# Kernel tuning notes

Measured on AMD Instinct MI355X. Metric: run time of the kernel, lower is better.

Reference implementation:

```python
import jax, jax.numpy as jnp
import numpy as np

SEG_NUM = 100000
D_SEG = 128
D_S = 258       # 2*D_SEG + 2 (offset)
D_M7 = 512
D_M8 = 256
MASK = 64
T_SLOTS = 96
B = 4096
CAND_OUT = 4            # candidate_layer out_features
DW_COLS = D_M8 - CAND_OUT  # 252
BN_EPS = 1e-6
COS_EPS = 1e-8


def setup_inputs() -> dict:
    key = jax.random.key(0)
    ks = jax.random.split(key, 20)
    s = 0.02
    return {
        "src": jax.random.randint(ks[0], (B,), 0, SEG_NUM),
        "dest": jax.random.randint(ks[1], (B,), 0, SEG_NUM),
        "t": jax.random.randint(ks[2], (B,), 0, T_SLOTS),
        "candidates": jax.random.randint(ks[3], (B, MASK), 0, SEG_NUM),
        "offset": jax.random.normal(ks[4], (B, 4), jnp.float32),
        "emb_feat": jax.random.normal(ks[5], (SEG_NUM, D_SEG), jnp.float32) * s,
        "emb_dest": jax.random.normal(ks[6], (SEG_NUM, D_SEG), jnp.float32) * s,
        "w1": jax.random.normal(ks[7], (D_M7, D_S), jnp.float32) * s,
        "b1": jnp.zeros((D_M7,), jnp.float32),
        "bn_gamma": jnp.ones((D_M7,), jnp.float32),
        "bn_beta": jnp.zeros((D_M7,), jnp.float32),
        "bn_mean": jax.random.normal(ks[8], (D_M7,), jnp.float32) * s,
        "bn_var": jax.random.uniform(ks[9], (D_M7,), jnp.float32, 0.5, 1.5),
        "w2": jax.random.normal(ks[10], (D_M8, D_M7), jnp.float32) * s,
        "b2": jnp.zeros((D_M8,), jnp.float32),
        "dense_w": jax.random.normal(ks[11], (SEG_NUM, DW_COLS), jnp.float32) * s,
        "dense_b": jnp.zeros((SEG_NUM,), jnp.float32),
        "cand_w": jax.random.normal(ks[12], (CAND_OUT, 2), jnp.float32) * s,
        "cand_b": jnp.zeros((CAND_OUT,), jnp.float32),
        "segs_src": jax.random.normal(ks[13], (SEG_NUM, 2), jnp.float32),
        "segs_trg": jax.random.normal(ks[14], (SEG_NUM, 2), jnp.float32),
        "traffic_pop": jax.random.uniform(ks[15], (SEG_NUM, T_SLOTS), jnp.float32),
    }


def reference(src, dest, t, candidates, offset, emb_feat, emb_dest, w1, b1,
              bn_gamma, bn_beta, bn_mean, bn_var, w2, b2, dense_w, dense_b,
              cand_w, cand_b, segs_src, segs_trg, traffic_pop):
    # --- ODEncoder: embedding gathers + offset features ---
    code = jnp.concatenate([emb_feat[src], emb_dest[dest], offset[:, 1:3]], axis=1)  # [B, 258]
    # --- MLP: Linear -> BatchNorm1d (eval, running stats) -> ReLU -> Linear ---
    h = code @ w1.T + b1
    h = (h - bn_mean) * (bn_gamma / jnp.sqrt(bn_var + BN_EPS)) + bn_beta
    h = jax.nn.relu(h)
    out = h @ w2.T + b2  # [B, 256]
    # --- gather dense rows by candidate index ---
    sub_w = dense_w[candidates]   # [B, M, 252]
    sub_b = dense_b[candidates]   # [B, M]
    # --- traffic feature: traffic_pop[candidate, t] ---
    traffic_feat = traffic_pop[candidates, t[:, None]]  # [B, M]
    # --- cosine similarity between dest-direction and segment direction ---
    v1 = segs_src[dest][:, None, :] - segs_src[candidates]  # [B, M, 2]
    v2 = segs_trg[candidates] - segs_src[candidates]        # [B, M, 2]
    num = jnp.sum(v1 * v2, axis=-1)
    den = jnp.maximum(jnp.linalg.norm(v1, axis=-1) * jnp.linalg.norm(v2, axis=-1), COS_EPS)
    cos_feat = num / den  # [B, M]
    cand_feat = jnp.stack([cos_feat, traffic_feat], axis=-1)  # [B, M, 2]
    emb_cand = cand_feat @ cand_w.T + cand_b                  # [B, M, 4]
    W = jnp.concatenate([sub_w, emb_cand], axis=-1)           # [B, M, 256]
    # --- batched small matvec + bias ---
    logits = jnp.einsum('bmd,bd->bm', W, out) + sub_b         # [B, M]
    return logits
```

## Files before the change

### kernel.cpp

```cpp
#include <hip/hip_runtime.h>


#define BATCH 4096
#define DSEG 128
#define DS_ 258
#define DM7 512
#define DM8 256
#define NCAND 64
#define DWC 252
#define TSLOTS 96

typedef short bf16x8 __attribute__((ext_vector_type(8)));
typedef float f32x4 __attribute__((ext_vector_type(4)));

static __device__ __forceinline__ short f2bf(float f) {
    union { float f; unsigned u; } v; v.f = f;
    unsigned r = (v.u + 0x7FFFu + ((v.u >> 16) & 1u)) >> 16;
    return (short)r;
}

__global__ __launch_bounds__(512) void mlp_mfma_kernel(
    const int* __restrict__ src, const int* __restrict__ dest,
    const float* __restrict__ offset,
    const float* __restrict__ emb_feat, const float* __restrict__ emb_dest,
    const float* __restrict__ w1, const float* __restrict__ b1,
    const float* __restrict__ bn_gamma, const float* __restrict__ bn_beta,
    const float* __restrict__ bn_mean, const float* __restrict__ bn_var,
    const float* __restrict__ w2, const float* __restrict__ b2,
    float* __restrict__ out_ws)
{
    __shared__ __align__(16) short hlds[16][520];
    const int tid = threadIdx.x;
    const int w    = tid >> 6;
    const int lane = tid & 63;
    const int lg   = lane >> 4;
    const int lr   = lane & 15;
    const int b0   = blockIdx.x * 16;

    const int si = src[b0 + lr];
    const int di = dest[b0 + lr];
    const float* fb = emb_feat + (size_t)si * DSEG;
    const float* db = emb_dest + (size_t)di * DSEG;
    bf16x8 a1[8];
#pragma unroll
    for (int s = 0; s < 8; ++s) {
        const float* p = (s < 4) ? (fb + s * 32 + lg * 8)
                                 : (db + (s - 4) * 32 + lg * 8);
        const float4 x = *(const float4*)p;
        const float4 y = *(const float4*)(p + 4);
        bf16x8 t;
        t[0] = f2bf(x.x); t[1] = f2bf(x.y); t[2] = f2bf(x.z); t[3] = f2bf(x.w);
        t[4] = f2bf(y.x); t[5] = f2bf(y.y); t[6] = f2bf(y.z); t[7] = f2bf(y.w);
        a1[s] = t;
    }
    float off1[4], off2[4];
#pragma unroll
    for (int q = 0; q < 4; ++q) {
        const float4 o = *(const float4*)(offset + (size_t)(b0 + lg * 4 + q) * 4);
        off1[q] = o.y; off2[q] = o.z;
    }

#pragma unroll
    for (int nt = 0; nt < 4; ++nt) {
        const int n = (w * 4 + nt) * 16 + lr;
        const float* wrow = w1 + (size_t)n * DS_;
        f32x4 acc = {0.f, 0.f, 0.f, 0.f};
#pragma unroll
        for (int s = 0; s < 8; ++s) {
            const float* p = wrow + s * 32 + lg * 8;
            const float2 x0 = *(const float2*)(p);
            const float2 x1 = *(const float2*)(p + 2);
            const float2 x2 = *(const float2*)(p + 4);
            const float2 x3 = *(const float2*)(p + 6);
            bf16x8 bb;
            bb[0] = f2bf(x0.x); bb[1] = f2bf(x0.y); bb[2] = f2bf(x1.x); bb[3] = f2bf(x1.y);
            bb[4] = f2bf(x2.x); bb[5] = f2bf(x2.y); bb[6] = f2bf(x3.x); bb[7] = f2bf(x3.y);
            acc = __builtin_amdgcn_mfma_f32_16x16x32_bf16(a1[s], bb, acc, 0, 0, 0);
        }
        const float2 wtail = *(const float2*)(wrow + 256);
        const float scale = bn_gamma[n] / sqrtf(bn_var[n] + 1e-6f);
        const float shift = bn_beta[n] - bn_mean[n] * scale;
        const float bias  = b1[n];
#pragma unroll
        for (int q = 0; q < 4; ++q) {
            float v = acc[q] + bias + off1[q] * wtail.x + off2[q] * wtail.y;
            v = fmaf(v, scale, shift);
            v = fmaxf(v, 0.f);
            hlds[lg * 4 + q][n] = f2bf(v);
        }
    }
    __syncthreads();

    bf16x8 a2[16];
#pragma unroll
    for (int s = 0; s < 16; ++s) {
        a2[s] = *(const bf16x8*)&hlds[lr][s * 32 + lg * 8];
    }
#pragma unroll
    for (int nt = 0; nt < 2; ++nt) {
        const int n = (w * 2 + nt) * 16 + lr;
        const float* wrow = w2 + (size_t)n * DM7;
        f32x4 acc = {0.f, 0.f, 0.f, 0.f};
#pragma unroll
        for (int s = 0; s < 16; ++s) {
            const float4 x = *(const float4*)(wrow + s * 32 + lg * 8);
            const float4 y = *(const float4*)(wrow + s * 32 + lg * 8 + 4);
            bf16x8 bb;
            bb[0] = f2bf(x.x); bb[1] = f2bf(x.y); bb[2] = f2bf(x.z); bb[3] = f2bf(x.w);
            bb[4] = f2bf(y.x); bb[5] = f2bf(y.y); bb[6] = f2bf(y.z); bb[7] = f2bf(y.w);
            acc = __builtin_amdgcn_mfma_f32_16x16x32_bf16(a2[s], bb, acc, 0, 0, 0);
        }
        const float bias = b2[n];
#pragma unroll
        for (int q = 0; q < 4; ++q) {
            out_ws[(size_t)(b0 + lg * 4 + q) * DM8 + n] = acc[q] + bias;
        }
    }
}

__global__ __launch_bounds__(256) void logits_kernel(
    const int* __restrict__ dest, const int* __restrict__ tt,
    const int* __restrict__ candidates,
    const float* __restrict__ dense_w, const float* __restrict__ dense_b,
    const float* __restrict__ cand_w, const float* __restrict__ cand_b,
    const float* __restrict__ segs_src, const float* __restrict__ segs_trg,
    const float* __restrict__ traffic_pop,
    const float* __restrict__ out_ws,
    float* __restrict__ logits)
{
    const int b = blockIdx.x;
    const int tid = threadIdx.x;
    const int wave = tid >> 6;
    const int lane = tid & 63;
    const int mbase = wave * 16;

    const int ll = (lane < 63) ? lane : 62;
    float4 o4 = *(const float4*)(out_ws + (size_t)b * DM8 + ll * 4);
    if (lane == 63) { o4.x = 0.f; o4.y = 0.f; o4.z = 0.f; o4.w = 0.f; }

    float tail = 0.f;
    int candv = 0;
    if (lane < 16) {
        const int m = mbase + lane;
        candv = candidates[b * NCAND + m];
        const float4 t4 = *(const float4*)(out_ws + (size_t)b * DM8 + DWC);
        const int db = dest[b];
        const float2 dsx = *(const float2*)(segs_src + 2 * (size_t)db);
        const float2 sx = *(const float2*)(segs_src + 2 * (size_t)candv);
        const float2 tx = *(const float2*)(segs_trg + 2 * (size_t)candv);
        const float v1x = dsx.x - sx.x, v1y = dsx.y - sx.y;
        const float v2x = tx.x - sx.x, v2y = tx.y - sx.y;
        const float num = v1x * v2x + v1y * v2y;
        const float den = fmaxf(sqrtf(v1x * v1x + v1y * v1y) *
                                sqrtf(v2x * v2x + v2y * v2y), 1e-8f);
        const float cosv = num / den;
        const float tf = traffic_pop[(size_t)candv * TSLOTS + tt[b]];
        const float e0 = fmaf(cosv, cand_w[0], fmaf(tf, cand_w[1], cand_b[0]));
        const float e1 = fmaf(cosv, cand_w[2], fmaf(tf, cand_w[3], cand_b[1]));
        const float e2 = fmaf(cosv, cand_w[4], fmaf(tf, cand_w[5], cand_b[2]));
        const float e3 = fmaf(cosv, cand_w[6], fmaf(tf, cand_w[7], cand_b[3]));
        tail = e0 * t4.x + e1 * t4.y + e2 * t4.z + e3 * t4.w + dense_b[candv];
    }

    for (int mi = 0; mi < 16; mi += 4) {
        const int c0 = __shfl(candv, mi + 0, 64);
        const int c1 = __shfl(candv, mi + 1, 64);
        const int c2 = __shfl(candv, mi + 2, 64);
        const int c3 = __shfl(candv, mi + 3, 64);
        const float4 dw0 = *(const float4*)(dense_w + (size_t)c0 * DWC + ll * 4);
        const float4 dw1 = *(const float4*)(dense_w + (size_t)c1 * DWC + ll * 4);
        const float4 dw2 = *(const float4*)(dense_w + (size_t)c2 * DWC + ll * 4);
        const float4 dw3 = *(const float4*)(dense_w + (size_t)c3 * DWC + ll * 4);
        float p0 = dw0.x * o4.x + dw0.y * o4.y + dw0.z * o4.z + dw0.w * o4.w;
        float p1 = dw1.x * o4.x + dw1.y * o4.y + dw1.z * o4.z + dw1.w * o4.w;
        float p2 = dw2.x * o4.x + dw2.y * o4.y + dw2.z * o4.z + dw2.w * o4.w;
        float p3 = dw3.x * o4.x + dw3.y * o4.y + dw3.z * o4.z + dw3.w * o4.w;
        const float t0 = __shfl(tail, mi + 0, 64);
        const float t1 = __shfl(tail, mi + 1, 64);
        const float t2 = __shfl(tail, mi + 2, 64);
        const float t3 = __shfl(tail, mi + 3, 64);
#pragma unroll
        for (int s = 1; s < 64; s <<= 1) {
            p0 += __shfl_xor(p0, s, 64);
            p1 += __shfl_xor(p1, s, 64);
            p2 += __shfl_xor(p2, s, 64);
            p3 += __shfl_xor(p3, s, 64);
        }
        if (lane == 0) {
            float4 res;
            res.x = p0 + t0; res.y = p1 + t1; res.z = p2 + t2; res.w = p3 + t3;
            *(float4*)(logits + (size_t)b * NCAND + mbase + mi) = res;
        }
    }
}

extern "C" void kernel_launch(void* const* d_in, const int* in_sizes, int n_in,
                              void* d_out, int out_size, void* d_ws, size_t ws_size,
                              hipStream_t stream) {
    const int*   src         = (const int*)d_in[0];
    const int*   dest        = (const int*)d_in[1];
    const int*   tt          = (const int*)d_in[2];
    const int*   candidates  = (const int*)d_in[3];
    const float* offset      = (const float*)d_in[4];
    const float* emb_feat    = (const float*)d_in[5];
    const float* emb_dest    = (const float*)d_in[6];
    const float* w1          = (const float*)d_in[7];
    const float* b1          = (const float*)d_in[8];
    const float* bn_gamma    = (const float*)d_in[9];
    const float* bn_beta     = (const float*)d_in[10];
    const float* bn_mean     = (const float*)d_in[11];
    const float* bn_var      = (const float*)d_in[12];
    const float* w2          = (const float*)d_in[13];
    const float* b2          = (const float*)d_in[14];
    const float* dense_w     = (const float*)d_in[15];
    const float* dense_b     = (const float*)d_in[16];
    const float* cand_w      = (const float*)d_in[17];
    const float* cand_b      = (const float*)d_in[18];
    const float* segs_src    = (const float*)d_in[19];
    const float* segs_trg    = (const float*)d_in[20];
    const float* traffic_pop = (const float*)d_in[21];

    float* out_ws = (float*)d_ws;
    float* logits = (float*)d_out;

    mlp_mfma_kernel<<<BATCH / 16, 512, 0, stream>>>(
        src, dest, offset, emb_feat, emb_dest,
        w1, b1, bn_gamma, bn_beta, bn_mean, bn_var, w2, b2, out_ws);

    logits_kernel<<<BATCH, 256, 0, stream>>>(
        dest, tt, candidates, dense_w, dense_b, cand_w, cand_b,
        segs_src, segs_trg, traffic_pop, out_ws, logits);
}
```

Before: 90.21 us.

## Issue all 16 dense_w row gathers upfront and reduce partials through LDS

The logits kernel now loads all 16 candidate dense_w rows per wave into registers before the dependent tail computation, so every gather is in flight at once instead of in groups of four. The butterfly shuffle reduction is replaced by writing per-lane partial dot products to a padded shared-memory array, followed by a 16-element strided sum per lane and two shuffles. This aims to raise memory-level parallelism on the random row gathers and cut shuffle instruction count. In exchange it uses 64 more VGPRs per thread, adds shared memory and a block-wide barrier, and may reduce occupancy.

Result: no change. 89.28 us (-1.0%).

```diff
diff --git a/kernel.cpp b/kernel.cpp
--- a/kernel.cpp
+++ b/kernel.cpp
@@ -128,21 +128,29 @@
     const float* __restrict__ out_ws,
     float* __restrict__ logits)
 {
+    __shared__ float plds[4][16][67];
     const int b = blockIdx.x;
     const int tid = threadIdx.x;
     const int wave = tid >> 6;
     const int lane = tid & 63;
     const int mbase = wave * 16;
 
+    int candv = 0;
+    if (lane < 16) candv = candidates[b * NCAND + mbase + lane];
+
     const int ll = (lane < 63) ? lane : 62;
+    float4 dw[16];
+#pragma unroll
+    for (int i = 0; i < 16; ++i) {
+        const int ci = __shfl(candv, i, 64);
+        dw[i] = *(const float4*)(dense_w + (size_t)ci * DWC + ll * 4);
+    }
+
     float4 o4 = *(const float4*)(out_ws + (size_t)b * DM8 + ll * 4);
     if (lane == 63) { o4.x = 0.f; o4.y = 0.f; o4.z = 0.f; o4.w = 0.f; }
 
     float tail = 0.f;
-    int candv = 0;
     if (lane < 16) {
-        const int m = mbase + lane;
-        candv = candidates[b * NCAND + m];
         const float4 t4 = *(const float4*)(out_ws + (size_t)b * DM8 + DWC);
         const int db = dest[b];
         const float2 dsx = *(const float2*)(segs_src + 2 * (size_t)db);
@@ -162,36 +170,22 @@
         tail = e0 * t4.x + e1 * t4.y + e2 * t4.z + e3 * t4.w + dense_b[candv];
     }
 
-    for (int mi = 0; mi < 16; mi += 4) {
-        const int c0 = __shfl(candv, mi + 0, 64);
-        const int c1 = __shfl(candv, mi + 1, 64);
-        const int c2 = __shfl(candv, mi + 2, 64);
-        const int c3 = __shfl(candv, mi + 3, 64);
-        const float4 dw0 = *(const float4*)(dense_w + (size_t)c0 * DWC + ll * 4);
-        const float4 dw1 = *(const float4*)(dense_w + (size_t)c1 * DWC + ll * 4);
-        const float4 dw2 = *(const float4*)(dense_w + (size_t)c2 * DWC + ll * 4);
-        const float4 dw3 = *(const float4*)(dense_w + (size_t)c3 * DWC + ll * 4);
-        float p0 = dw0.x * o4.x + dw0.y * o4.y + dw0.z * o4.z + dw0.w * o4.w;
-        float p1 = dw1.x * o4.x + dw1.y * o4.y + dw1.z * o4.z + dw1.w * o4.w;
-        float p2 = dw2.x * o4.x + dw2.y * o4.y + dw2.z * o4.z + dw2.w * o4.w;
-        float p3 = dw3.x * o4.x + dw3.y * o4.y + dw3.z * o4.z + dw3.w * o4.w;
-        const float t0 = __shfl(tail, mi + 0, 64);
-        const float t1 = __shfl(tail, mi + 1, 64);
-        const float t2 = __shfl(tail, mi + 2, 64);
-        const float t3 = __shfl(tail, mi + 3, 64);
-#pragma unroll
-        for (int s = 1; s < 64; s <<= 1) {
-            p0 += __shfl_xor(p0, s, 64);
-            p1 += __shfl_xor(p1, s, 64);
-            p2 += __shfl_xor(p2, s, 64);
-            p3 += __shfl_xor(p3, s, 64);
-        }
-        if (lane == 0) {
-            float4 res;
-            res.x = p0 + t0; res.y = p1 + t1; res.z = p2 + t2; res.w = p3 + t3;
-            *(float4*)(logits + (size_t)b * NCAND + mbase + mi) = res;
-        }
-    }
+#pragma unroll
+    for (int i = 0; i < 16; ++i) {
+        const float p = dw[i].x * o4.x + dw[i].y * o4.y + dw[i].z * o4.z + dw[i].w * o4.w;
+        plds[wave][i][lane] = p;
+    }
+    __syncthreads();
+
+    const int cc = lane >> 2;
+    const int qq = lane & 3;
+    float s = 0.f;
+#pragma unroll
+    for (int j = 0; j < 16; ++j) s += plds[wave][cc][qq * 16 + j];
+    s += __shfl_xor(s, 1, 64);
+    s += __shfl_xor(s, 2, 64);
+    const float tl = __shfl(tail, cc, 64);
+    if (qq == 0) logits[(size_t)b * NCAND + mbase + cc] = s + tl;
 }
 
 extern "C" void kernel_launch(void* const* d_in, const int* in_sizes, int n_in,
```
